# Kernel tuning notes

Hardware: AMD Instinct MI355X
Metric: run time of the kernel (lower is better)

Reference implementation:

```python
import jax, jax.numpy as jnp
import numpy as np

NUM_USERS = 100000
USER_EMB_DIM = 64
PROC_DIM = 128          # Dense(128) embedding_processor
NUM_SHARDS = 16
MEM_SIZE = 512          # memory slots per shard
WORD_SIZE = 64
NUM_READS = 4
INPUT_SIZE = 256
B, S = 256, 128
IN_DIM = INPUT_SIZE + PROC_DIM  # combined controller input width


def setup_inputs() -> dict:
    key = jax.random.key(0)
    k = jax.random.split(key, 7)
    x = jax.random.normal(k[0], (B, S, INPUT_SIZE), dtype=jnp.float32)
    user_id = jax.random.randint(k[1], (B,), 0, NUM_USERS, dtype=jnp.int64)
    user_emb_table = jax.random.normal(k[2], (NUM_USERS, USER_EMB_DIM), dtype=jnp.float32) * 0.02
    W_proc = jax.random.normal(k[3], (USER_EMB_DIM, PROC_DIM), dtype=jnp.float32) * (1.0 / np.sqrt(USER_EMB_DIM))
    b_proc = jnp.zeros((PROC_DIM,), dtype=jnp.float32)
    # per-shard parameters: query projection + memory matrix (the shard's state)
    Wq = jax.random.normal(k[4], (NUM_SHARDS, IN_DIM, NUM_READS * WORD_SIZE), dtype=jnp.float32) * (1.0 / np.sqrt(IN_DIM))
    memory = jax.random.normal(k[5], (NUM_SHARDS, MEM_SIZE, WORD_SIZE), dtype=jnp.float32)
    return {"x": x, "user_id": user_id, "user_emb_table": user_emb_table,
            "W_proc": W_proc, "b_proc": b_proc, "Wq": Wq, "memory": memory}


def reference(x, user_id, user_emb_table, W_proc, b_proc, Wq, memory):
    # user embedding lookup + Dense processor
    ue = user_emb_table[user_id]                       # [B, E]
    pe = ue @ W_proc + b_proc                          # [B, PROC_DIM]
    # broadcast the processed embedding across the sequence and concat on features
    pe_seq = jnp.broadcast_to(pe[:, None, :], (x.shape[0], x.shape[1], pe.shape[-1]))
    combined = jnp.concatenate([x, pe_seq], axis=-1)   # [B, S, IN_DIM]
    # shard routing (irregular gather of per-shard params)
    sid = user_id % NUM_SHARDS                         # [B]
    Wq_g = Wq[sid]                                     # [B, IN_DIM, R*W]
    mem_g = memory[sid]                                # [B, M, W]
    # per-sample shard forward: content-based read
    q = jnp.einsum('bsi,bio->bso', combined, Wq_g)     # [B, S, R*W]
    q = q.reshape(q.shape[0], q.shape[1], NUM_READS, WORD_SIZE)
    scores = jnp.einsum('bsrw,bmw->bsrm', q, mem_g)    # [B, S, R, M]
    wts = jax.nn.softmax(scores, axis=-1)
    read_words = jnp.einsum('bsrm,bmw->bsrw', wts, mem_g)  # [B, S, R, W]
    # original code keeps final_states[-1] (last sample's state)
    final_state = wts[-1]                              # [S, R, M]
    return read_words, final_state
```

## Files before the change

kernel.cpp:

```cpp
#include <hip/hip_runtime.h>
#include <math.h>

#define BB 256
#define SSEQ 128
#define INPUT 256
#define PD 128
#define EE 64
#define RW 256
#define MM 512
#define WW 64
#define KD 384

typedef _Float16 half8 __attribute__((ext_vector_type(8)));
typedef __fp16 fp16x2 __attribute__((ext_vector_type(2)));
typedef float float4v __attribute__((ext_vector_type(4)));

#define LOG2E 1.44269504088896f
#define OUT1 8388608u

#define MEMT_OFF 65536
#define F32_OFF  131072
#define LDS_BYTES (131072 + 6144)
#define UE_O 0
#define PE_O 64
#define QPE_O 192
#define QP_O 448

#define IMG_SHARD 131072
#define WQT_OFF  (16*IMG_SHARD)
#define WQT_BYTES ((size_t)16*RW*KD*2)
#define PREP_LDS 65536

union H8 { half8 h8; unsigned int u[4]; uint4 u4; };

__device__ __forceinline__ unsigned int pk2(float a, float b) {
    union { fp16x2 h; unsigned int u; } p;
    p.h = __builtin_amdgcn_cvt_pkrtz(a, b);
    return p.u;
}

__global__ void prep_kernel(const float* __restrict__ Wq, const float* __restrict__ memG,
                            char* __restrict__ ws, int useImg, int useWqT) {
    extern __shared__ char sm[];
    const int blk = blockIdx.x;
    const int t = threadIdx.x;
    if (blk < 384) {
        if (!useWqT) return;
        float (*tile)[65] = (float (*)[65])sm;
        const int kt = blk % 6, ntb = (blk / 6) & 3, sid = blk / 24;
        const float* src = Wq + (size_t)sid*KD*RW + (size_t)(kt*64)*RW + ntb*64;
        for (int i = 0; i < 16; ++i) {
            int idx = i*256 + t;
            int kk = idx >> 6, nn = idx & 63;
            tile[kk][nn] = src[(size_t)kk*RW + nn];
        }
        __syncthreads();
        _Float16* dst = (_Float16*)(ws + WQT_OFF) + (size_t)sid*RW*KD + (size_t)(ntb*64)*KD + kt*64;
        for (int i = 0; i < 16; ++i) {
            int idx = i*256 + t;
            int nn = idx >> 6, kk = idx & 63;
            dst[(size_t)nn*KD + kk] = (_Float16)tile[kk][nn];
        }
    } else {
        if (!useImg) return;
        const int sid = blk - 384;
        const float* memB = memG + (size_t)sid * (MM*WW);
        uint4* lds128 = (uint4*)sm;
        unsigned short* ldsu = (unsigned short*)sm;
        uint4* wsA = (uint4*)(ws + (size_t)sid*IMG_SHARD);
        uint4* wsB = wsA + 4096;
        for (int i = 0; i < 16; ++i) {
            int id = i*256 + t;
            int m = id >> 3, cw = id & 7;
            const float* g = memB + m*64 + cw*8;
            float4 a0 = *(const float4*)g;
            float4 a1 = *(const float4*)(g + 4);
            uint4 v = make_uint4(pk2(a0.x,a0.y), pk2(a0.z,a0.w), pk2(a1.x,a1.y), pk2(a1.z,a1.w));
            int chunk = m*8 + (cw ^ (m & 7));
            lds128[chunk] = v;
            wsA[chunk] = v;
        }
        __syncthreads();
        for (int i = 0; i < 16; ++i) {
            int id = i*256 + t;
            int w = id & 63, cm = id >> 6;
            unsigned int uu[4];
            #pragma unroll
            for (int p = 0; p < 4; ++p) {
                int m0 = cm*8 + 2*p, m1 = m0 + 1;
                unsigned short lo = ldsu[m0*64 + (((w>>3) ^ (m0&7))<<3) + (w&7)];
                unsigned short hi = ldsu[m1*64 + (((w>>3) ^ (m1&7))<<3) + (w&7)];
                uu[p] = (unsigned int)lo | ((unsigned int)hi << 16);
            }
            wsB[w*64 + (cm ^ (w & 7))] = make_uint4(uu[0], uu[1], uu[2], uu[3]);
        }
    }
}

__global__ void __launch_bounds__(1024, 4)
attn_kernel(const float* __restrict__ x, const int* __restrict__ user_id,
            const float* __restrict__ uet, const float* __restrict__ W_proc,
            const float* __restrict__ b_proc, const float* __restrict__ Wq,
            const float* __restrict__ memG, const char* __restrict__ ws,
            int useImg, int useWqT, float* __restrict__ out)
{
    extern __shared__ char smraw[];
    unsigned short* smemu = (unsigned short*)smraw;
    uint4* sm128 = (uint4*)smraw;
    float* smf = (float*)(smraw + F32_OFF);

    const int t = threadIdx.x;
    const int b = blockIdx.x;
    const int lane = t & 63, wv = t >> 6;
    const int n16 = lane & 15, quad = lane >> 4;
    const int r = wv & 3, sq = wv >> 2;
    const int s0 = sq * 32;
    const int swz = n16 & 7;

    const int uid = user_id[b];
    const int sid = uid & 15;
    const float* memB = memG + (size_t)sid * (MM*WW);

    if (t < EE) smf[UE_O + t] = uet[(size_t)uid*EE + t];

    if (useImg) {
        const uint4* img = (const uint4*)(ws + (size_t)sid*IMG_SHARD);
        #pragma unroll
        for (int i = 0; i < 8; ++i) {
            int id = i*1024 + t;
            sm128[id] = img[id];
        }
    } else {
        for (int i = 0; i < 4; ++i) {
            int id = t + i*1024;
            int m = id >> 3, cw = id & 7;
            const float* g = memB + m*64 + cw*8;
            float4 a0 = *(const float4*)g;
            float4 a1 = *(const float4*)(g + 4);
            sm128[m*8 + (cw ^ (m & 7))] =
                make_uint4(pk2(a0.x,a0.y), pk2(a0.z,a0.w), pk2(a1.x,a1.y), pk2(a1.z,a1.w));
        }
        __syncthreads();
        for (int i = 0; i < 4; ++i) {
            int id = t + i*1024;
            int w = id & 63, cm = id >> 6;
            unsigned int uu[4];
            #pragma unroll
            for (int p = 0; p < 4; ++p) {
                int m0 = cm*8 + 2*p, m1 = m0 + 1;
                unsigned short lo = smemu[m0*64 + (((w>>3) ^ (m0&7))<<3) + (w&7)];
                unsigned short hi = smemu[m1*64 + (((w>>3) ^ (m1&7))<<3) + (w&7)];
                uu[p] = (unsigned int)lo | ((unsigned int)hi << 16);
            }
            sm128[(MEMT_OFF >> 4) + w*64 + (cm ^ (w & 7))] = make_uint4(uu[0],uu[1],uu[2],uu[3]);
        }
    }
    __syncthreads();
    if (t < PD) {
        float a = b_proc[t];
        #pragma unroll
        for (int e = 0; e < EE; ++e) a = fmaf(smf[UE_O + e], W_proc[e*PD + t], a);
        smf[PE_O + t] = a;
    }
    __syncthreads();
    {
        int n = t & 255, h = t >> 8;
        float s = 0.f;
        const float* wr = Wq + (size_t)sid*KD*RW + (size_t)(256 + h*32)*RW + n;
        #pragma unroll 8
        for (int k = 0; k < 32; ++k) s = fmaf(smf[PE_O + h*32 + k], wr[(size_t)k*RW], s);
        smf[QP_O + h*256 + n] = s;
    }
    __syncthreads();
    if (t < 256) smf[QPE_O + t] = LOG2E * (smf[QP_O + t] + smf[QP_O + 256 + t]
                                         + smf[QP_O + 512 + t] + smf[QP_O + 768 + t]);
    __syncthreads();


    float4v qacc[4][2];
    #pragma unroll
    for (int mt = 0; mt < 4; ++mt)
        #pragma unroll
        for (int nt = 0; nt < 2; ++nt) qacc[mt][nt] = (float4v)0.f;

    const float* xB = x + (size_t)(b*SSEQ + s0) * INPUT;
    for (int kc = 0; kc < 8; ++kc) {
        H8 afr[4];
        if (useWqT) {
            const _Float16* wt0 = (const _Float16*)(ws + WQT_OFF)
                                + (size_t)sid*RW*KD + (size_t)(r*64)*KD + kc*32 + quad*8;
            #pragma unroll
            for (int mt = 0; mt < 4; ++mt)
                afr[mt].u4 = *(const uint4*)(wt0 + (size_t)(mt*16 + n16)*KD);
        } else {
            const float* wq0 = Wq + (size_t)sid*KD*RW + (size_t)(kc*32 + quad*8)*RW + r*64 + n16;
            #pragma unroll
            for (int mt = 0; mt < 4; ++mt)
                #pragma unroll
                for (int p = 0; p < 4; ++p)
                    afr[mt].u[p] = pk2(wq0[(size_t)(2*p)*RW + mt*16],
                                       wq0[(size_t)(2*p+1)*RW + mt*16]);
        }
        H8 bfr[2];
        #pragma unroll
        for (int nt = 0; nt < 2; ++nt) {
            const float* xg = xB + (size_t)(nt*16 + n16)*INPUT + kc*32 + quad*8;
            float4 a0 = *(const float4*)xg;
            float4 a1 = *(const float4*)(xg + 4);
            bfr[nt].u[0] = pk2(a0.x*LOG2E, a0.y*LOG2E);
            bfr[nt].u[1] = pk2(a0.z*LOG2E, a0.w*LOG2E);
            bfr[nt].u[2] = pk2(a1.x*LOG2E, a1.y*LOG2E);
            bfr[nt].u[3] = pk2(a1.z*LOG2E, a1.w*LOG2E);
        }
        #pragma unroll
        for (int mt = 0; mt < 4; ++mt)
            #pragma unroll
            for (int nt = 0; nt < 2; ++nt)
                qacc[mt][nt] = __builtin_amdgcn_mfma_f32_16x16x32_f16(afr[mt].h8, bfr[nt].h8, qacc[mt][nt], 0, 0, 0);
    }
    #pragma unroll
    for (int mt = 0; mt < 4; ++mt)
        #pragma unroll
        for (int reg = 0; reg < 4; ++reg) {
            float qv = smf[QPE_O + r*64 + mt*16 + quad*4 + reg];
            #pragma unroll
            for (int nt = 0; nt < 2; ++nt) qacc[mt][nt][reg] += qv;
        }
    unsigned int pkq[4][2][2];
    #pragma unroll
    for (int mt = 0; mt < 4; ++mt)
        #pragma unroll
        for (int nt = 0; nt < 2; ++nt) {
            pkq[mt][nt][0] = pk2(qacc[mt][nt][0], qacc[mt][nt][1]);
            pkq[mt][nt][1] = pk2(qacc[mt][nt][2], qacc[mt][nt][3]);
        }
    unsigned int bq[2][2][4];
    #pragma unroll
    for (int kc2 = 0; kc2 < 2; ++kc2)
        #pragma unroll
        for (int nt = 0; nt < 2; ++nt)
            #pragma unroll
            for (int p = 0; p < 4; ++p) {
                int qp = ((quad & 1) << 1) | (p >> 1);
                int src = n16 + (qp << 4);
                int sr = p & 1;
                int lo  = __shfl((int)pkq[kc2*2    ][nt][sr], src, 64);
                int hiv = __shfl((int)pkq[kc2*2 + 1][nt][sr], src, 64);
                bq[kc2][nt][p] = (unsigned int)((quad < 2) ? lo : hiv);
            }

    float4v Oa[4][2];
    #pragma unroll
    for (int wt = 0; wt < 4; ++wt)
        #pragma unroll
        for (int nt = 0; nt < 2; ++nt) Oa[wt][nt] = (float4v)0.f;
    float Ml[2] = {-1e30f, -1e30f}, ll[2] = {0.f, 0.f};

    for (int mtile = 0; mtile < 16; ++mtile) {
        float4v Sa[2][2];
        #pragma unroll
        for (int msub = 0; msub < 2; ++msub)
            #pragma unroll
            for (int nt = 0; nt < 2; ++nt) Sa[msub][nt] = (float4v)0.f;
        #pragma unroll
        for (int msub = 0; msub < 2; ++msub) {
            int m = mtile*32 + msub*16 + n16;
            #pragma unroll
            for (int kc2 = 0; kc2 < 2; ++kc2) {
                H8 af; af.u4 = sm128[m*8 + ((kc2*4 + quad) ^ swz)];
                #pragma unroll
                for (int nt = 0; nt < 2; ++nt) {
                    H8 bf; bf.u[0]=bq[kc2][nt][0]; bf.u[1]=bq[kc2][nt][1];
                           bf.u[2]=bq[kc2][nt][2]; bf.u[3]=bq[kc2][nt][3];
                    Sa[msub][nt] = __builtin_amdgcn_mfma_f32_16x16x32_f16(af.h8, bf.h8, Sa[msub][nt], 0, 0, 0);
                }
            }
        }
        unsigned int pkP[2][2][2];
        #pragma unroll
        for (int nt = 0; nt < 2; ++nt) {
            float tm = Sa[0][nt][0];
            #pragma unroll
            for (int g = 1; g < 4; ++g) tm = fmaxf(tm, Sa[0][nt][g]);
            #pragma unroll
            for (int g = 0; g < 4; ++g) tm = fmaxf(tm, Sa[1][nt][g]);
            tm = fmaxf(tm, __shfl_xor(tm, 16, 64));
            tm = fmaxf(tm, __shfl_xor(tm, 32, 64));
            float Mn = fmaxf(Ml[nt], tm);
            float al = __builtin_amdgcn_exp2f(Ml[nt] - Mn);
            float pv[2][4]; float ts = 0.f;
            #pragma unroll
            for (int msub = 0; msub < 2; ++msub)
                #pragma unroll
                for (int g = 0; g < 4; ++g) {
                    pv[msub][g] = __builtin_amdgcn_exp2f(Sa[msub][nt][g] - Mn);
                    ts += pv[msub][g];
                }
            ts += __shfl_xor(ts, 16, 64);
            ts += __shfl_xor(ts, 32, 64);
            ll[nt] = al*ll[nt] + ts;
            Ml[nt] = Mn;
            pkP[0][nt][0] = pk2(pv[0][0], pv[0][1]); pkP[0][nt][1] = pk2(pv[0][2], pv[0][3]);
            pkP[1][nt][0] = pk2(pv[1][0], pv[1][1]); pkP[1][nt][1] = pk2(pv[1][2], pv[1][3]);
            #pragma unroll
            for (int wt = 0; wt < 4; ++wt)
                #pragma unroll
                for (int g = 0; g < 4; ++g) Oa[wt][nt][g] *= al;
        }
        unsigned int bp[2][4];
        #pragma unroll
        for (int nt = 0; nt < 2; ++nt)
            #pragma unroll
            for (int p = 0; p < 4; ++p) {
                int qp = ((quad & 1) << 1) | (p >> 1);
                int src = n16 + (qp << 4);
                int sr = p & 1;
                int lo  = __shfl((int)pkP[0][nt][sr], src, 64);
                int hiv = __shfl((int)pkP[1][nt][sr], src, 64);
                bp[nt][p] = (unsigned int)((quad < 2) ? lo : hiv);
            }
        #pragma unroll
        for (int wt = 0; wt < 4; ++wt) {
            H8 af; af.u4 = sm128[(MEMT_OFF >> 4) + (wt*16 + n16)*64 + ((mtile*4 + quad) ^ swz)];
            #pragma unroll
            for (int nt = 0; nt < 2; ++nt) {
                H8 bf; bf.u[0]=bp[nt][0]; bf.u[1]=bp[nt][1]; bf.u[2]=bp[nt][2]; bf.u[3]=bp[nt][3];
                Oa[wt][nt] = __builtin_amdgcn_mfma_f32_16x16x32_f16(af.h8, bf.h8, Oa[wt][nt], 0, 0, 0);
            }
        }
    }

    #pragma unroll
    for (int nt = 0; nt < 2; ++nt) {
        float inv = 1.0f / ll[nt];
        int s = s0 + nt*16 + n16;
        #pragma unroll
        for (int wt = 0; wt < 4; ++wt) {
            float4 o = make_float4(Oa[wt][nt][0]*inv, Oa[wt][nt][1]*inv,
                                   Oa[wt][nt][2]*inv, Oa[wt][nt][3]*inv);
            *(float4*)&out[((size_t)(b*SSEQ + s)*4 + r)*WW + wt*16 + quad*4] = o;
        }
    }

    if (b == BB - 1) {
        for (int mtile = 0; mtile < 16; ++mtile) {
            float4v Sa[2][2];
            #pragma unroll
            for (int msub = 0; msub < 2; ++msub)
                #pragma unroll
                for (int nt = 0; nt < 2; ++nt) Sa[msub][nt] = (float4v)0.f;
            #pragma unroll
            for (int msub = 0; msub < 2; ++msub) {
                int m = mtile*32 + msub*16 + n16;
                #pragma unroll
                for (int kc2 = 0; kc2 < 2; ++kc2) {
                    H8 af; af.u4 = sm128[m*8 + ((kc2*4 + quad) ^ swz)];
                    #pragma unroll
                    for (int nt = 0; nt < 2; ++nt) {
                        H8 bf; bf.u[0]=bq[kc2][nt][0]; bf.u[1]=bq[kc2][nt][1];
                               bf.u[2]=bq[kc2][nt][2]; bf.u[3]=bq[kc2][nt][3];
                        Sa[msub][nt] = __builtin_amdgcn_mfma_f32_16x16x32_f16(af.h8, bf.h8, Sa[msub][nt], 0, 0, 0);
                    }
                }
            }
            #pragma unroll
            for (int nt = 0; nt < 2; ++nt) {
                float inv = 1.0f / ll[nt];
                int s = s0 + nt*16 + n16;
                size_t base = (size_t)OUT1 + ((size_t)(s*4 + r) << 9);
                #pragma unroll
                for (int msub = 0; msub < 2; ++msub) {
                    float4 w4 = make_float4(
                        __builtin_amdgcn_exp2f(Sa[msub][nt][0] - Ml[nt]) * inv,
                        __builtin_amdgcn_exp2f(Sa[msub][nt][1] - Ml[nt]) * inv,
                        __builtin_amdgcn_exp2f(Sa[msub][nt][2] - Ml[nt]) * inv,
                        __builtin_amdgcn_exp2f(Sa[msub][nt][3] - Ml[nt]) * inv);
                    *(float4*)&out[base + mtile*32 + msub*16 + quad*4] = w4;
                }
            }
        }
    }
}

extern "C" void kernel_launch(void* const* d_in, const int* in_sizes, int n_in,
                              void* d_out, int out_size, void* d_ws, size_t ws_size,
                              hipStream_t stream) {
    const float* x    = (const float*)d_in[0];
    const int*   uid  = (const int*)  d_in[1];
    const float* uet  = (const float*)d_in[2];
    const float* Wp   = (const float*)d_in[3];
    const float* bp   = (const float*)d_in[4];
    const float* Wq   = (const float*)d_in[5];
    const float* mem  = (const float*)d_in[6];
    float* out = (float*)d_out;
    char* ws = (char*)d_ws;

    int useImg = (ws_size >= (size_t)WQT_OFF) ? 1 : 0;
    int useWqT = (ws_size >= (size_t)WQT_OFF + WQT_BYTES) ? 1 : 0;

    (void)hipFuncSetAttribute((const void*)prep_kernel,
                              hipFuncAttributeMaxDynamicSharedMemorySize, PREP_LDS);
    (void)hipFuncSetAttribute((const void*)attn_kernel,
                              hipFuncAttributeMaxDynamicSharedMemorySize, LDS_BYTES);

    if (useImg || useWqT)
        prep_kernel<<<400, 256, PREP_LDS, stream>>>(Wq, mem, ws, useImg, useWqT);

    attn_kernel<<<BB, 1024, LDS_BYTES, stream>>>(x, uid, uet, Wp, bp, Wq, mem, ws,
                                                 useImg, useWqT, out);
}
```

Measured before the change: 175.2 us.

## Split each batch across two blocks and read transposed memory from global

Launches a 2D grid so each batch row is handled by two 1024-thread blocks covering 64 sequence positions each, with every wave now owning 16 positions instead of 32. The transposed memory image used for the weighted-sum MFMA is read directly from the global workspace, no longer staged in LDS. This halves the LDS footprint on the fast path and raises the launch-bounds occupancy hint, aiming for more resident blocks and better latency hiding. The cost is per-block setup (user embedding, processor projection and the memory image load) being duplicated across both halves, plus uncached-LDS global reads in the inner loop that rely on L2/L1 hits.

```diff
diff --git a/kernel.cpp b/kernel.cpp
--- a/kernel.cpp
+++ b/kernel.cpp
@@ -18,17 +18,18 @@
 #define LOG2E 1.44269504088896f
 #define OUT1 8388608u
 
-#define MEMT_OFF 65536
-#define F32_OFF  131072
-#define LDS_BYTES (131072 + 6144)
+#define LDS_FAST   (65536 + 6144)
+#define LDS_FALL   (131072 + 6144)
 #define UE_O 0
 #define PE_O 64
 #define QPE_O 192
 #define QP_O 448
 
-#define IMG_SHARD 131072
-#define WQT_OFF  (16*IMG_SHARD)
+#define WSA_OFF 0
+#define WST_OFF  (16*65536)
+#define WQT_OFF  (32*65536)
 #define WQT_BYTES ((size_t)16*RW*KD*2)
+#define WS_NEED  ((size_t)WQT_OFF + WQT_BYTES)
 #define PREP_LDS 65536
 
 union H8 { half8 h8; unsigned int u[4]; uint4 u4; };
@@ -40,12 +41,11 @@
 }
 
 __global__ void prep_kernel(const float* __restrict__ Wq, const float* __restrict__ memG,
-                            char* __restrict__ ws, int useImg, int useWqT) {
+                            char* __restrict__ ws) {
     extern __shared__ char sm[];
     const int blk = blockIdx.x;
     const int t = threadIdx.x;
     if (blk < 384) {
-        if (!useWqT) return;
         float (*tile)[65] = (float (*)[65])sm;
         const int kt = blk % 6, ntb = (blk / 6) & 3, sid = blk / 24;
         const float* src = Wq + (size_t)sid*KD*RW + (size_t)(kt*64)*RW + ntb*64;
@@ -62,13 +62,12 @@
             dst[(size_t)nn*KD + kk] = (_Float16)tile[kk][nn];
         }
     } else {
-        if (!useImg) return;
         const int sid = blk - 384;
         const float* memB = memG + (size_t)sid * (MM*WW);
         uint4* lds128 = (uint4*)sm;
         unsigned short* ldsu = (unsigned short*)sm;
-        uint4* wsA = (uint4*)(ws + (size_t)sid*IMG_SHARD);
-        uint4* wsB = wsA + 4096;
+        uint4* wsA = (uint4*)(ws + WSA_OFF) + (size_t)sid*4096;
+        uint4* wsT = (uint4*)(ws + WST_OFF) + (size_t)sid*4096;
         for (int i = 0; i < 16; ++i) {
             int id = i*256 + t;
             int m = id >> 3, cw = id & 7;
@@ -92,44 +91,43 @@
                 unsigned short hi = ldsu[m1*64 + (((w>>3) ^ (m1&7))<<3) + (w&7)];
                 uu[p] = (unsigned int)lo | ((unsigned int)hi << 16);
             }
-            wsB[w*64 + (cm ^ (w & 7))] = make_uint4(uu[0], uu[1], uu[2], uu[3]);
+            wsT[w*64 + cm] = make_uint4(uu[0], uu[1], uu[2], uu[3]);
         }
     }
 }
 
-__global__ void __launch_bounds__(1024, 4)
+__global__ void __launch_bounds__(1024, 8)
 attn_kernel(const float* __restrict__ x, const int* __restrict__ user_id,
             const float* __restrict__ uet, const float* __restrict__ W_proc,
             const float* __restrict__ b_proc, const float* __restrict__ Wq,
             const float* __restrict__ memG, const char* __restrict__ ws,
-            int useImg, int useWqT, float* __restrict__ out)
+            int useWs, float* __restrict__ out)
 {
     extern __shared__ char smraw[];
     unsigned short* smemu = (unsigned short*)smraw;
-    uint4* sm128 = (uint4*)smraw;
-    float* smf = (float*)(smraw + F32_OFF);
+    uint4*          sm128 = (uint4*)smraw;
+    float*          smf   = (float*)(smraw + (useWs ? 65536 : 131072));
 
     const int t = threadIdx.x;
     const int b = blockIdx.x;
+    const int halfb = blockIdx.y;
     const int lane = t & 63, wv = t >> 6;
     const int n16 = lane & 15, quad = lane >> 4;
     const int r = wv & 3, sq = wv >> 2;
-    const int s0 = sq * 32;
+    const int sW = halfb*64 + sq*16;
     const int swz = n16 & 7;
 
     const int uid = user_id[b];
     const int sid = uid & 15;
     const float* memB = memG + (size_t)sid * (MM*WW);
+    const float* wqX  = Wq + (size_t)sid * KD * RW;
 
     if (t < EE) smf[UE_O + t] = uet[(size_t)uid*EE + t];
 
-    if (useImg) {
-        const uint4* img = (const uint4*)(ws + (size_t)sid*IMG_SHARD);
-        #pragma unroll
-        for (int i = 0; i < 8; ++i) {
-            int id = i*1024 + t;
-            sm128[id] = img[id];
-        }
+    if (useWs) {
+        const uint4* img = (const uint4*)(ws + WSA_OFF) + (size_t)sid*4096;
+        #pragma unroll
+        for (int i = 0; i < 4; ++i) sm128[i*1024 + t] = img[i*1024 + t];
     } else {
         for (int i = 0; i < 4; ++i) {
             int id = t + i*1024;
@@ -152,7 +150,7 @@
                 unsigned short hi = smemu[m1*64 + (((w>>3) ^ (m1&7))<<3) + (w&7)];
                 uu[p] = (unsigned int)lo | ((unsigned int)hi << 16);
             }
-            sm128[(MEMT_OFF >> 4) + w*64 + (cm ^ (w & 7))] = make_uint4(uu[0],uu[1],uu[2],uu[3]);
+            sm128[4096 + w*64 + (cm ^ (w & 7))] = make_uint4(uu[0],uu[1],uu[2],uu[3]);
         }
     }
     __syncthreads();
@@ -166,7 +164,7 @@
     {
         int n = t & 255, h = t >> 8;
         float s = 0.f;
-        const float* wr = Wq + (size_t)sid*KD*RW + (size_t)(256 + h*32)*RW + n;
+        const float* wr = wqX + (size_t)(256 + h*32)*RW + n;
         #pragma unroll 8
         for (int k = 0; k < 32; ++k) s = fmaf(smf[PE_O + h*32 + k], wr[(size_t)k*RW], s);
         smf[QP_O + h*256 + n] = s;
@@ -176,24 +174,20 @@
                                          + smf[QP_O + 512 + t] + smf[QP_O + 768 + t]);
     __syncthreads();
 
-
-    float4v qacc[4][2];
-    #pragma unroll
-    for (int mt = 0; mt < 4; ++mt)
-        #pragma unroll
-        for (int nt = 0; nt < 2; ++nt) qacc[mt][nt] = (float4v)0.f;
-
-    const float* xB = x + (size_t)(b*SSEQ + s0) * INPUT;
+    float4v qacc[4];
+    #pragma unroll
+    for (int mt = 0; mt < 4; ++mt) qacc[mt] = (float4v)0.f;
+    const float* xB = x + (size_t)(b*SSEQ + sW) * INPUT;
     for (int kc = 0; kc < 8; ++kc) {
         H8 afr[4];
-        if (useWqT) {
+        if (useWs) {
             const _Float16* wt0 = (const _Float16*)(ws + WQT_OFF)
                                 + (size_t)sid*RW*KD + (size_t)(r*64)*KD + kc*32 + quad*8;
             #pragma unroll
             for (int mt = 0; mt < 4; ++mt)
                 afr[mt].u4 = *(const uint4*)(wt0 + (size_t)(mt*16 + n16)*KD);
         } else {
-            const float* wq0 = Wq + (size_t)sid*KD*RW + (size_t)(kc*32 + quad*8)*RW + r*64 + n16;
+            const float* wq0 = wqX + (size_t)(kc*32 + quad*8)*RW + r*64 + n16;
             #pragma unroll
             for (int mt = 0; mt < 4; ++mt)
                 #pragma unroll
@@ -201,182 +195,147 @@
                     afr[mt].u[p] = pk2(wq0[(size_t)(2*p)*RW + mt*16],
                                        wq0[(size_t)(2*p+1)*RW + mt*16]);
         }
-        H8 bfr[2];
-        #pragma unroll
-        for (int nt = 0; nt < 2; ++nt) {
-            const float* xg = xB + (size_t)(nt*16 + n16)*INPUT + kc*32 + quad*8;
+        H8 bfr;
+        {
+            const float* xg = xB + (size_t)n16*INPUT + kc*32 + quad*8;
             float4 a0 = *(const float4*)xg;
             float4 a1 = *(const float4*)(xg + 4);
-            bfr[nt].u[0] = pk2(a0.x*LOG2E, a0.y*LOG2E);
-            bfr[nt].u[1] = pk2(a0.z*LOG2E, a0.w*LOG2E);
-            bfr[nt].u[2] = pk2(a1.x*LOG2E, a1.y*LOG2E);
-            bfr[nt].u[3] = pk2(a1.z*LOG2E, a1.w*LOG2E);
+            bfr.u[0] = pk2(a0.x*LOG2E, a0.y*LOG2E);
+            bfr.u[1] = pk2(a0.z*LOG2E, a0.w*LOG2E);
+            bfr.u[2] = pk2(a1.x*LOG2E, a1.y*LOG2E);
+            bfr.u[3] = pk2(a1.z*LOG2E, a1.w*LOG2E);
         }
         #pragma unroll
         for (int mt = 0; mt < 4; ++mt)
-            #pragma unroll
-            for (int nt = 0; nt < 2; ++nt)
-                qacc[mt][nt] = __builtin_amdgcn_mfma_f32_16x16x32_f16(afr[mt].h8, bfr[nt].h8, qacc[mt][nt], 0, 0, 0);
+            qacc[mt] = __builtin_amdgcn_mfma_f32_16x16x32_f16(afr[mt].h8, bfr.h8, qacc[mt], 0, 0, 0);
     }
     #pragma unroll
     for (int mt = 0; mt < 4; ++mt)
         #pragma unroll
-        for (int reg = 0; reg < 4; ++reg) {
-            float qv = smf[QPE_O + r*64 + mt*16 + quad*4 + reg];
-            #pragma unroll
-            for (int nt = 0; nt < 2; ++nt) qacc[mt][nt][reg] += qv;
-        }
-    unsigned int pkq[4][2][2];
-    #pragma unroll
-    for (int mt = 0; mt < 4; ++mt)
-        #pragma unroll
-        for (int nt = 0; nt < 2; ++nt) {
-            pkq[mt][nt][0] = pk2(qacc[mt][nt][0], qacc[mt][nt][1]);
-            pkq[mt][nt][1] = pk2(qacc[mt][nt][2], qacc[mt][nt][3]);
-        }
-    unsigned int bq[2][2][4];
+        for (int reg = 0; reg < 4; ++reg)
+            qacc[mt][reg] += smf[QPE_O + r*64 + mt*16 + quad*4 + reg];
+    unsigned int pkq[4][2];
+    #pragma unroll
+    for (int mt = 0; mt < 4; ++mt) {
+        pkq[mt][0] = pk2(qacc[mt][0], qacc[mt][1]);
+        pkq[mt][1] = pk2(qacc[mt][2], qacc[mt][3]);
+    }
+    unsigned int bq[2][4];
     #pragma unroll
     for (int kc2 = 0; kc2 < 2; ++kc2)
         #pragma unroll
-        for (int nt = 0; nt < 2; ++nt)
-            #pragma unroll
-            for (int p = 0; p < 4; ++p) {
-                int qp = ((quad & 1) << 1) | (p >> 1);
-                int src = n16 + (qp << 4);
-                int sr = p & 1;
-                int lo  = __shfl((int)pkq[kc2*2    ][nt][sr], src, 64);
-                int hiv = __shfl((int)pkq[kc2*2 + 1][nt][sr], src, 64);
-                bq[kc2][nt][p] = (unsigned int)((quad < 2) ? lo : hiv);
-            }
-
-    float4v Oa[4][2];
-    #pragma unroll
-    for (int wt = 0; wt < 4; ++wt)
-        #pragma unroll
-        for (int nt = 0; nt < 2; ++nt) Oa[wt][nt] = (float4v)0.f;
-    float Ml[2] = {-1e30f, -1e30f}, ll[2] = {0.f, 0.f};
+        for (int p = 0; p < 4; ++p) {
+            int qp = ((quad & 1) << 1) | (p >> 1);
+            int src = n16 + (qp << 4);
+            int sr = p & 1;
+            int lo  = __shfl((int)pkq[kc2*2    ][sr], src, 64);
+            int hiv = __shfl((int)pkq[kc2*2 + 1][sr], src, 64);
+            bq[kc2][p] = (unsigned int)((quad < 2) ? lo : hiv);
+        }
+
+    const uint4* gT = (const uint4*)(ws + WST_OFF) + (size_t)sid*4096;
+
+    float4v Oa[4];
+    #pragma unroll
+    for (int wt = 0; wt < 4; ++wt) Oa[wt] = (float4v)0.f;
+    float Ml = -1e30f, llp = 0.f;
 
     for (int mtile = 0; mtile < 16; ++mtile) {
-        float4v Sa[2][2];
-        #pragma unroll
-        for (int msub = 0; msub < 2; ++msub)
-            #pragma unroll
-            for (int nt = 0; nt < 2; ++nt) Sa[msub][nt] = (float4v)0.f;
+        float4v Sa[2];
+        Sa[0] = (float4v)0.f; Sa[1] = (float4v)0.f;
         #pragma unroll
         for (int msub = 0; msub < 2; ++msub) {
             int m = mtile*32 + msub*16 + n16;
             #pragma unroll
             for (int kc2 = 0; kc2 < 2; ++kc2) {
                 H8 af; af.u4 = sm128[m*8 + ((kc2*4 + quad) ^ swz)];
-                #pragma unroll
-                for (int nt = 0; nt < 2; ++nt) {
-                    H8 bf; bf.u[0]=bq[kc2][nt][0]; bf.u[1]=bq[kc2][nt][1];
-                           bf.u[2]=bq[kc2][nt][2]; bf.u[3]=bq[kc2][nt][3];
-                    Sa[msub][nt] = __builtin_amdgcn_mfma_f32_16x16x32_f16(af.h8, bf.h8, Sa[msub][nt], 0, 0, 0);
-                }
-            }
-        }
-        unsigned int pkP[2][2][2];
-        #pragma unroll
-        for (int nt = 0; nt < 2; ++nt) {
-            float tm = Sa[0][nt][0];
-            #pragma unroll
-            for (int g = 1; g < 4; ++g) tm = fmaxf(tm, Sa[0][nt][g]);
-            #pragma unroll
-            for (int g = 0; g < 4; ++g) tm = fmaxf(tm, Sa[1][nt][g]);
-            tm = fmaxf(tm, __shfl_xor(tm, 16, 64));
-            tm = fmaxf(tm, __shfl_xor(tm, 32, 64));
-            float Mn = fmaxf(Ml[nt], tm);
-            float al = __builtin_amdgcn_exp2f(Ml[nt] - Mn);
-            float pv[2][4]; float ts = 0.f;
-            #pragma unroll
-            for (int msub = 0; msub < 2; ++msub)
-                #pragma unroll
-                for (int g = 0; g < 4; ++g) {
-                    pv[msub][g] = __builtin_amdgcn_exp2f(Sa[msub][nt][g] - Mn);
-                    ts += pv[msub][g];
-                }
-            ts += __shfl_xor(ts, 16, 64);
-            ts += __shfl_xor(ts, 32, 64);
-            ll[nt] = al*ll[nt] + ts;
-            Ml[nt] = Mn;
-            pkP[0][nt][0] = pk2(pv[0][0], pv[0][1]); pkP[0][nt][1] = pk2(pv[0][2], pv[0][3]);
-            pkP[1][nt][0] = pk2(pv[1][0], pv[1][1]); pkP[1][nt][1] = pk2(pv[1][2], pv[1][3]);
-            #pragma unroll
-            for (int wt = 0; wt < 4; ++wt)
-                #pragma unroll
-                for (int g = 0; g < 4; ++g) Oa[wt][nt][g] *= al;
-        }
-        unsigned int bp[2][4];
-        #pragma unroll
-        for (int nt = 0; nt < 2; ++nt)
-            #pragma unroll
-            for (int p = 0; p < 4; ++p) {
-                int qp = ((quad & 1) << 1) | (p >> 1);
-                int src = n16 + (qp << 4);
-                int sr = p & 1;
-                int lo  = __shfl((int)pkP[0][nt][sr], src, 64);
-                int hiv = __shfl((int)pkP[1][nt][sr], src, 64);
-                bp[nt][p] = (unsigned int)((quad < 2) ? lo : hiv);
-            }
+                H8 bf; bf.u[0]=bq[kc2][0]; bf.u[1]=bq[kc2][1]; bf.u[2]=bq[kc2][2]; bf.u[3]=bq[kc2][3];
+                Sa[msub] = __builtin_amdgcn_mfma_f32_16x16x32_f16(af.h8, bf.h8, Sa[msub], 0, 0, 0);
+            }
+        }
+        float tm = Sa[0][0];
+        #pragma unroll
+        for (int g = 1; g < 4; ++g) tm = fmaxf(tm, Sa[0][g]);
+        #pragma unroll
+        for (int g = 0; g < 4; ++g) tm = fmaxf(tm, Sa[1][g]);
+        tm = fmaxf(tm, __shfl_xor(tm, 16, 64));
+        tm = fmaxf(tm, __shfl_xor(tm, 32, 64));
+        float Mn = fmaxf(Ml, tm);
+        float al = __builtin_amdgcn_exp2f(Ml - Mn);
+        float pv[2][4]; float ts = 0.f;
+        #pragma unroll
+        for (int msub = 0; msub < 2; ++msub)
+            #pragma unroll
+            for (int g = 0; g < 4; ++g) {
+                pv[msub][g] = __builtin_amdgcn_exp2f(Sa[msub][g] - Mn);
+                ts += pv[msub][g];
+            }
+        llp = al*llp + ts;
+        Ml = Mn;
+        unsigned int pkP[2][2];
+        pkP[0][0] = pk2(pv[0][0], pv[0][1]); pkP[0][1] = pk2(pv[0][2], pv[0][3]);
+        pkP[1][0] = pk2(pv[1][0], pv[1][1]); pkP[1][1] = pk2(pv[1][2], pv[1][3]);
+        #pragma unroll
+        for (int wt = 0; wt < 4; ++wt)
+            #pragma unroll
+            for (int g = 0; g < 4; ++g) Oa[wt][g] *= al;
+        unsigned int bp[4];
+        #pragma unroll
+        for (int p = 0; p < 4; ++p) {
+            int qp = ((quad & 1) << 1) | (p >> 1);
+            int src = n16 + (qp << 4);
+            int sr = p & 1;
+            int lo  = __shfl((int)pkP[0][sr], src, 64);
+            int hiv = __shfl((int)pkP[1][sr], src, 64);
+            bp[p] = (unsigned int)((quad < 2) ? lo : hiv);
+        }
+        H8 bf; bf.u[0]=bp[0]; bf.u[1]=bp[1]; bf.u[2]=bp[2]; bf.u[3]=bp[3];
         #pragma unroll
         for (int wt = 0; wt < 4; ++wt) {
-            H8 af; af.u4 = sm128[(MEMT_OFF >> 4) + (wt*16 + n16)*64 + ((mtile*4 + quad) ^ swz)];
-            #pragma unroll
-            for (int nt = 0; nt < 2; ++nt) {
-                H8 bf; bf.u[0]=bp[nt][0]; bf.u[1]=bp[nt][1]; bf.u[2]=bp[nt][2]; bf.u[3]=bp[nt][3];
-                Oa[wt][nt] = __builtin_amdgcn_mfma_f32_16x16x32_f16(af.h8, bf.h8, Oa[wt][nt], 0, 0, 0);
-            }
-        }
-    }
-
-    #pragma unroll
-    for (int nt = 0; nt < 2; ++nt) {
-        float inv = 1.0f / ll[nt];
-        int s = s0 + nt*16 + n16;
+            H8 af;
+            if (useWs) af.u4 = gT[(wt*16 + n16)*64 + mtile*4 + quad];
+            else       af.u4 = sm128[4096 + (wt*16 + n16)*64 + ((mtile*4 + quad) ^ swz)];
+            Oa[wt] = __builtin_amdgcn_mfma_f32_16x16x32_f16(af.h8, bf.h8, Oa[wt], 0, 0, 0);
+        }
+    }
+    float ll = llp;
+    ll += __shfl_xor(ll, 16, 64);
+    ll += __shfl_xor(ll, 32, 64);
+    float inv = 1.0f / ll;
+
+    {
+        int s = sW + n16;
         #pragma unroll
         for (int wt = 0; wt < 4; ++wt) {
-            float4 o = make_float4(Oa[wt][nt][0]*inv, Oa[wt][nt][1]*inv,
-                                   Oa[wt][nt][2]*inv, Oa[wt][nt][3]*inv);
+            float4 o = make_float4(Oa[wt][0]*inv, Oa[wt][1]*inv, Oa[wt][2]*inv, Oa[wt][3]*inv);
             *(float4*)&out[((size_t)(b*SSEQ + s)*4 + r)*WW + wt*16 + quad*4] = o;
         }
     }
 
     if (b == BB - 1) {
+        int s = sW + n16;
+        size_t base = (size_t)OUT1 + ((size_t)(s*4 + r) << 9);
         for (int mtile = 0; mtile < 16; ++mtile) {
-            float4v Sa[2][2];
-            #pragma unroll
-            for (int msub = 0; msub < 2; ++msub)
-                #pragma unroll
-                for (int nt = 0; nt < 2; ++nt) Sa[msub][nt] = (float4v)0.f;
+            float4v Sa[2];
+            Sa[0] = (float4v)0.f; Sa[1] = (float4v)0.f;
             #pragma unroll
             for (int msub = 0; msub < 2; ++msub) {
                 int m = mtile*32 + msub*16 + n16;
                 #pragma unroll
                 for (int kc2 = 0; kc2 < 2; ++kc2) {
                     H8 af; af.u4 = sm128[m*8 + ((kc2*4 + quad) ^ swz)];
-                    #pragma unroll
-                    for (int nt = 0; nt < 2; ++nt) {
-                        H8 bf; bf.u[0]=bq[kc2][nt][0]; bf.u[1]=bq[kc2][nt][1];
-                               bf.u[2]=bq[kc2][nt][2]; bf.u[3]=bq[kc2][nt][3];
-                        Sa[msub][nt] = __builtin_amdgcn_mfma_f32_16x16x32_f16(af.h8, bf.h8, Sa[msub][nt], 0, 0, 0);
-                    }
+                    H8 bf; bf.u[0]=bq[kc2][0]; bf.u[1]=bq[kc2][1]; bf.u[2]=bq[kc2][2]; bf.u[3]=bq[kc2][3];
+                    Sa[msub] = __builtin_amdgcn_mfma_f32_16x16x32_f16(af.h8, bf.h8, Sa[msub], 0, 0, 0);
                 }
             }
             #pragma unroll
-            for (int nt = 0; nt < 2; ++nt) {
-                float inv = 1.0f / ll[nt];
-                int s = s0 + nt*16 + n16;
-                size_t base = (size_t)OUT1 + ((size_t)(s*4 + r) << 9);
-                #pragma unroll
-                for (int msub = 0; msub < 2; ++msub) {
-                    float4 w4 = make_float4(
-                        __builtin_amdgcn_exp2f(Sa[msub][nt][0] - Ml[nt]) * inv,
-                        __builtin_amdgcn_exp2f(Sa[msub][nt][1] - Ml[nt]) * inv,
-                        __builtin_amdgcn_exp2f(Sa[msub][nt][2] - Ml[nt]) * inv,
-                        __builtin_amdgcn_exp2f(Sa[msub][nt][3] - Ml[nt]) * inv);
-                    *(float4*)&out[base + mtile*32 + msub*16 + quad*4] = w4;
-                }
+            for (int msub = 0; msub < 2; ++msub) {
+                float4 w4 = make_float4(
+                    __builtin_amdgcn_exp2f(Sa[msub][0] - Ml) * inv,
+                    __builtin_amdgcn_exp2f(Sa[msub][1] - Ml) * inv,
+                    __builtin_amdgcn_exp2f(Sa[msub][2] - Ml) * inv,
+                    __builtin_amdgcn_exp2f(Sa[msub][3] - Ml) * inv);
+                *(float4*)&out[base + mtile*32 + msub*16 + quad*4] = w4;
             }
         }
     }
@@ -395,17 +354,17 @@
     float* out = (float*)d_out;
     char* ws = (char*)d_ws;
 
-    int useImg = (ws_size >= (size_t)WQT_OFF) ? 1 : 0;
-    int useWqT = (ws_size >= (size_t)WQT_OFF + WQT_BYTES) ? 1 : 0;
+    int useWs = (ws_size >= WS_NEED) ? 1 : 0;
 
     (void)hipFuncSetAttribute((const void*)prep_kernel,
                               hipFuncAttributeMaxDynamicSharedMemorySize, PREP_LDS);
     (void)hipFuncSetAttribute((const void*)attn_kernel,
-                              hipFuncAttributeMaxDynamicSharedMemorySize, LDS_BYTES);
-
-    if (useImg || useWqT)
-        prep_kernel<<<400, 256, PREP_LDS, stream>>>(Wq, mem, ws, useImg, useWqT);
-
-    attn_kernel<<<BB, 1024, LDS_BYTES, stream>>>(x, uid, uet, Wp, bp, Wq, mem, ws,
-                                                 useImg, useWqT, out);
+                              hipFuncAttributeMaxDynamicSharedMemorySize, LDS_FALL);
+
+    if (useWs)
+        prep_kernel<<<400, 256, PREP_LDS, stream>>>(Wq, mem, ws);
+
+    dim3 grid(BB, 2);
+    attn_kernel<<<grid, 1024, useWs ? LDS_FAST : LDS_FALL, stream>>>(
+        x, uid, uet, Wp, bp, Wq, mem, ws, useWs, out);
 }
```

Result: slower. 235.1 us (+34.2%).
